# Kernel tuning notes

Hardware: AMD Instinct MI355X
Metric: run time of the kernel (lower is better)

The kernel has to match this reference:

```python
import jax, jax.numpy as jnp
import numpy as np

EMBED_SIZE = 1024
HEADS = 16
HEAD_DIM = EMBED_SIZE // HEADS


def setup_inputs() -> dict:
    key = jax.random.key(0)
    ks = jax.random.split(key, 8)
    B, S = 4, 2048
    inp = {
        "values": jax.random.normal(ks[0], (B, S, EMBED_SIZE), dtype=jnp.float32),
        "keys": jax.random.normal(ks[1], (B, S, EMBED_SIZE), dtype=jnp.float32),
        "query": jax.random.normal(ks[2], (B, S, EMBED_SIZE), dtype=jnp.float32),
        "mask": jnp.zeros((B, S), dtype=jnp.int32),  # accepted but unused, as in the original
        # per-head projection weights (nn.Linear(head_dim, head_dim, bias=False)): y = x @ W.T
        "Wv": jax.random.normal(ks[3], (HEAD_DIM, HEAD_DIM), dtype=jnp.float32) / np.sqrt(HEAD_DIM),
        "Wk": jax.random.normal(ks[4], (HEAD_DIM, HEAD_DIM), dtype=jnp.float32) / np.sqrt(HEAD_DIM),
        "Wq": jax.random.normal(ks[5], (HEAD_DIM, HEAD_DIM), dtype=jnp.float32) / np.sqrt(HEAD_DIM),
        # fc_out: nn.Linear(embed_size, embed_size)
        "Wo": jax.random.normal(ks[6], (EMBED_SIZE, EMBED_SIZE), dtype=jnp.float32) / np.sqrt(EMBED_SIZE),
        "bo": jax.random.normal(ks[7], (EMBED_SIZE,), dtype=jnp.float32) * 0.01,
    }
    return inp


def reference(values, keys, query, mask, Wv, Wk, Wq, Wo, bo):
    N, S, _ = query.shape
    # reshape to (N, len, heads, head_dim)
    v = values.reshape(N, S, HEADS, HEAD_DIM)
    k = keys.reshape(N, S, HEADS, HEAD_DIM)
    q = query.reshape(N, S, HEADS, HEAD_DIM)
    # per-head linear projections (shared across heads), y = x @ W.T
    v = jnp.einsum('nlhd,ed->nlhe', v, Wv)
    k = jnp.einsum('nlhd,ed->nlhe', k, Wk)
    q = jnp.einsum('nlhd,ed->nlhe', q, Wq)
    # attention scores: (N, H, Q, K), scaled by sqrt(embed_size) as in the original
    energy = jnp.einsum('nqhd,nkhd->nhqk', q, k)
    attention = jax.nn.softmax(energy / jnp.sqrt(jnp.float32(EMBED_SIZE)), axis=3)
    out = jnp.einsum('nhql,nlhd->nqhd', attention, v).reshape(N, S, EMBED_SIZE)
    out = out @ Wo.T + bo
    return out
```

## Files before the change

### kernel.cpp

```cpp
#include <hip/hip_runtime.h>


typedef __attribute__((ext_vector_type(8))) short short8;
typedef __attribute__((ext_vector_type(4))) float f32x4;
typedef __attribute__((ext_vector_type(2))) unsigned int uint2v;

constexpr int Bn = 4, Sn = 2048, Hn = 16, Dn = 64, En = 1024;
constexpr int HEADELEMS = Bn * Hn * Sn * Dn;

__device__ __forceinline__ unsigned short f2bf(float f) {
  union { float f; unsigned u; } x; x.f = f;
  unsigned u = x.u;
  return (unsigned short)((u + 0x7FFFu + ((u >> 16) & 1u)) >> 16);
}

__device__ __forceinline__ short8 pack8(f32x4 a, f32x4 b) {
  short8 r;
  r[0] = (short)f2bf(a[0]); r[1] = (short)f2bf(a[1]);
  r[2] = (short)f2bf(a[2]); r[3] = (short)f2bf(a[3]);
  r[4] = (short)f2bf(b[0]); r[5] = (short)f2bf(b[1]);
  r[6] = (short)f2bf(b[2]); r[7] = (short)f2bf(b[3]);
  return r;
}

__device__ __forceinline__ float fexp2(float x) {
#if __has_builtin(__builtin_amdgcn_exp2f)
  return __builtin_amdgcn_exp2f(x);
#else
  return exp2f(x);
#endif
}

__device__ __forceinline__ unsigned cvtpk_bf16(float lo, float hi) {
  unsigned r;
  asm("v_cvt_pk_bf16_f32 %0, %1, %2" : "=v"(r) : "v"(lo), "v"(hi));
  return r;
}

__device__ __forceinline__ void gload_lds16(const unsigned short* g, unsigned short* l) {
  __builtin_amdgcn_global_load_lds((const __attribute__((address_space(1))) void*)g,
                                   (__attribute__((address_space(3))) void*)l, 16, 0, 0);
}

__global__ __launch_bounds__(256) void wfused_kernel(
    const float* __restrict__ Wq, const float* __restrict__ Wk,
    const float* __restrict__ Wv, const float* __restrict__ Wo,
    unsigned short* __restrict__ Ut, unsigned short* __restrict__ Mg) {
  __shared__ float lv[4096];
  const int e = blockIdx.x, t = threadIdx.x;
  for (int i = t; i < 4096; i += 256) lv[i] = Wv[i];
  __syncthreads();
#pragma unroll
  for (int i = 0; i < 4; ++i) {
    int hd = i * 256 + t;
    int h = hd >> 6, d = hd & 63;
    float acc = 0.f;
    const float* wrow = Wo + e * 1024 + h * 64;
    for (int dp = 0; dp < 64; ++dp) acc += lv[dp * 64 + d] * wrow[dp];
    Ut[e * 1024 + hd] = f2bf(acc);
  }
  if (e < 16) {
    int idx = e * 256 + t;
    int d = idx >> 6, c = idx & 63;
    float acc = 0.f;
    for (int o = 0; o < 64; ++o) acc += Wq[o * 64 + d] * Wk[o * 64 + c];
    Mg[idx] = f2bf(acc * 0.04508422f);
  }
}

__global__ __launch_bounds__(256) void prep_kernel(
    const float* __restrict__ vin, const float* __restrict__ kin,
    const unsigned short* __restrict__ Mg,
    unsigned short* __restrict__ kp, unsigned short* __restrict__ vT) {
  __shared__ alignas(16) unsigned short ldsK[64][72];
  __shared__ alignas(16) unsigned short ldsV[64][72];

  const int blk = blockIdx.x;
  const int st = blk & 31, h = (blk >> 5) & 15, b = blk >> 9;
  const int s0 = st * 64;
  const int t = threadIdx.x;
  const int wid = t >> 6, lane = t & 63, lg = lane >> 4, li = lane & 15;
  const int row = t >> 2, seg = t & 3;
  const int srcoff = (b * Sn + s0 + row) * En + h * 64 + seg * 16;

  {
    const f32x4* ks = reinterpret_cast<const f32x4*>(kin + srcoff);
    *reinterpret_cast<short8*>(&ldsK[row][seg * 16]) = pack8(ks[0], ks[1]);
    *reinterpret_cast<short8*>(&ldsK[row][seg * 16 + 8]) = pack8(ks[2], ks[3]);
    const f32x4* vs = reinterpret_cast<const f32x4*>(vin + srcoff);
    *reinterpret_cast<short8*>(&ldsV[row][seg * 16]) = pack8(vs[0], vs[1]);
    *reinterpret_cast<short8*>(&ldsV[row][seg * 16 + 8]) = pack8(vs[2], vs[3]);
  }
  __syncthreads();

  {
    const int d = lane, sq = wid;
    unsigned short col[16];
#pragma unroll
    for (int j = 0; j < 16; ++j) col[j] = ldsV[sq * 16 + j][d];
    short8 o0, o1;
#pragma unroll
    for (int j = 0; j < 8; ++j) { o0[j] = (short)col[j]; o1[j] = (short)col[8 + j]; }
    unsigned short* dst = vT + ((size_t)((b * Hn + h) * Dn + d)) * Sn + s0 + sq * 16;
    *reinterpret_cast<short8*>(dst) = o0;
    *reinterpret_cast<short8*>(dst + 8) = o1;
  }

  {
    short8 ka0 = *reinterpret_cast<const short8*>(&ldsK[wid * 16 + li][lg * 8]);
    short8 ka1 = *reinterpret_cast<const short8*>(&ldsK[wid * 16 + li][32 + lg * 8]);
    f32x4 acc[4] = {{0,0,0,0},{0,0,0,0},{0,0,0,0},{0,0,0,0}};
#pragma unroll
    for (int cb = 0; cb < 4; ++cb) {
      short8 b0 = *reinterpret_cast<const short8*>(Mg + (cb * 16 + li) * 64 + lg * 8);
      short8 b1 = *reinterpret_cast<const short8*>(Mg + (cb * 16 + li) * 64 + 32 + lg * 8);
      acc[cb] = __builtin_amdgcn_mfma_f32_16x16x32_bf16(ka0, b0, acc[cb], 0, 0, 0);
      acc[cb] = __builtin_amdgcn_mfma_f32_16x16x32_bf16(ka1, b1, acc[cb], 0, 0, 0);
    }
#pragma unroll
    for (int cb = 0; cb < 4; ++cb)
#pragma unroll
      for (int r = 0; r < 4; ++r)
        ldsK[wid * 16 + lg * 4 + r][cb * 16 + li] = f2bf(acc[cb][r]);
  }
  __syncthreads();

  {
    unsigned short* dst = kp + ((size_t)((b * Hn + h) * Sn + s0 + row)) * Dn + seg * 16;
    *reinterpret_cast<short8*>(dst) = *reinterpret_cast<const short8*>(&ldsK[row][seg * 16]);
    *reinterpret_cast<short8*>(dst + 8) = *reinterpret_cast<const short8*>(&ldsK[row][seg * 16 + 8]);
  }
}

__global__ __launch_bounds__(512, 4) void attn_kernel(
    const float* __restrict__ qin, const unsigned short* __restrict__ kp,
    const unsigned short* __restrict__ vT, unsigned short* __restrict__ pv) {
  __shared__ alignas(16) unsigned short ldsK[2][4096];
  __shared__ alignas(16) unsigned short ldsV[2][4096];
  __shared__ alignas(16) unsigned short ldsP[8][32][72];

  const int bid = blockIdx.x;
  const int xcd = bid & 7, j = bid >> 3;
  const int bh = ((j & 7) << 3) + xcd;
  const int qt = j >> 3;
  const int b = bh >> 4, h = bh & 15;

  const int t = threadIdx.x;
  const int wid = t >> 6, lane = t & 63, lg = lane >> 4, li = lane & 15;
  const int bhS = bh * Sn;
  const int q0 = qt * 256 + wid * 32;

  const int koff0 = ((lg ^ (li & 7)) << 3);

  const int sr = t >> 3, sg = t & 7;
  const unsigned short* ksrc = kp + (size_t)(bhS + sr) * Dn + ((sg ^ (sr & 7)) << 3);
  const unsigned short* vsrc = vT + ((size_t)bh * Dn + sr) * Sn + ((sg ^ (sr & 7)) << 3);

  short8 qb[2][2];
#pragma unroll
  for (int rb = 0; rb < 2; ++rb)
#pragma unroll
    for (int kc = 0; kc < 2; ++kc) {
      const float* qrow = qin + (size_t)(b * Sn + q0 + rb * 16 + li) * En + h * 64 + kc * 32 + lg * 8;
      f32x4 a = *reinterpret_cast<const f32x4*>(qrow);
      f32x4 c = *reinterpret_cast<const f32x4*>(qrow + 4);
      qb[rb][kc] = pack8(a, c);
    }

  f32x4 o[2][4];
#pragma unroll
  for (int rb = 0; rb < 2; ++rb)
#pragma unroll
    for (int i = 0; i < 4; ++i) o[rb][i] = f32x4{0, 0, 0, 0};
  float l0 = 0.f, l1 = 0.f;

  auto stage = [&](int buf, int kt) {
    gload_lds16(ksrc + (size_t)kt * 4096, &ldsK[buf][t * 8]);
    gload_lds16(vsrc + kt * 64, &ldsV[buf][t * 8]);
  };

  stage(0, 0);
  __syncthreads();
  int cur = 0;

  for (int kt = 0; kt < 32; ++kt) {
    if (kt < 31) stage(cur ^ 1, kt + 1);

    const unsigned short* Kb = ldsK[cur];
#pragma unroll
    for (int cb = 0; cb < 4; ++cb) {
      const int ra = (cb * 16 + li) * 64 + koff0;
      short8 ka0 = *reinterpret_cast<const short8*>(&Kb[ra]);
      short8 ka1 = *reinterpret_cast<const short8*>(&Kb[ra ^ 32]);
      f32x4 s0 = {0, 0, 0, 0}, s1 = {0, 0, 0, 0};
      s0 = __builtin_amdgcn_mfma_f32_16x16x32_bf16(ka0, qb[0][0], s0, 0, 0, 0);
      s0 = __builtin_amdgcn_mfma_f32_16x16x32_bf16(ka1, qb[0][1], s0, 0, 0, 0);
      s1 = __builtin_amdgcn_mfma_f32_16x16x32_bf16(ka0, qb[1][0], s1, 0, 0, 0);
      s1 = __builtin_amdgcn_mfma_f32_16x16x32_bf16(ka1, qb[1][1], s1, 0, 0, 0);
      float p0[4], p1[4];
#pragma unroll
      for (int r = 0; r < 4; ++r) {
        p0[r] = fexp2(s0[r]); l0 += p0[r];
        p1[r] = fexp2(s1[r]); l1 += p1[r];
      }
      uint2v w0, w1;
      w0[0] = cvtpk_bf16(p0[0], p0[1]); w0[1] = cvtpk_bf16(p0[2], p0[3]);
      w1[0] = cvtpk_bf16(p1[0], p1[1]); w1[1] = cvtpk_bf16(p1[2], p1[3]);
      *reinterpret_cast<uint2v*>(&ldsP[wid][li][cb * 16 + 4 * lg]) = w0;
      *reinterpret_cast<uint2v*>(&ldsP[wid][16 + li][cb * 16 + 4 * lg]) = w1;
    }

    short8 pa[2][2];
#pragma unroll
    for (int rb = 0; rb < 2; ++rb)
#pragma unroll
      for (int kc = 0; kc < 2; ++kc)
        pa[rb][kc] = *reinterpret_cast<const short8*>(
            &ldsP[wid][rb * 16 + li][kc * 32 + lg * 8]);

    const unsigned short* Vb = ldsV[cur];
#pragma unroll
    for (int db = 0; db < 4; ++db) {
      const int va = (db * 16 + li) * 64 + koff0;
      short8 vb0 = *reinterpret_cast<const short8*>(&Vb[va]);
      short8 vb1 = *reinterpret_cast<const short8*>(&Vb[va ^ 32]);
      o[0][db] = __builtin_amdgcn_mfma_f32_16x16x32_bf16(pa[0][0], vb0, o[0][db], 0, 0, 0);
      o[0][db] = __builtin_amdgcn_mfma_f32_16x16x32_bf16(pa[0][1], vb1, o[0][db], 0, 0, 0);
      o[1][db] = __builtin_amdgcn_mfma_f32_16x16x32_bf16(pa[1][0], vb0, o[1][db], 0, 0, 0);
      o[1][db] = __builtin_amdgcn_mfma_f32_16x16x32_bf16(pa[1][1], vb1, o[1][db], 0, 0, 0);
    }

    __syncthreads();
    cur ^= 1;
  }

  l0 += __shfl_xor(l0, 16, 64); l0 += __shfl_xor(l0, 32, 64);
  l1 += __shfl_xor(l1, 16, 64); l1 += __shfl_xor(l1, 32, 64);
#pragma unroll
  for (int r = 0; r < 4; ++r) {
    float i0 = 1.f / __shfl(l0, 4 * lg + r, 16);
    float i1 = 1.f / __shfl(l1, 4 * lg + r, 16);
    const int sg2 = q0 + 4 * lg + r;
    unsigned short* d0 = pv + ((size_t)(b * Sn + sg2) * Hn + h) * Dn + li;
    unsigned short* d1 = d0 + (size_t)16 * Hn * Dn;
#pragma unroll
    for (int db = 0; db < 4; ++db) {
      d0[db * 16] = f2bf(o[0][db][r] * i0);
      d1[db * 16] = f2bf(o[1][db][r] * i1);
    }
  }
}

__global__ __launch_bounds__(256) void ogemm_kernel(
    const unsigned short* __restrict__ pvm, const unsigned short* __restrict__ Ut,
    const float* __restrict__ bo, float* __restrict__ out) {
  __shared__ alignas(16) unsigned short ldsA[2][8192];
  __shared__ alignas(16) unsigned short ldsB[2][8192];

  const int bid = blockIdx.x;
  const int wg = (bid & 7) * 64 + (bid >> 3);
  const int en = wg & 7, mt = wg >> 3;
  const int t = threadIdx.x;
  const int wid = t >> 6, lane = t & 63, lg = lane >> 4, li = lane & 15;
  const int wr = wid >> 1, wc = wid & 1;
  const int m0 = mt * 128, e0 = en * 128;

  f32x4 acc[4][4];
#pragma unroll
  for (int i = 0; i < 4; ++i)
#pragma unroll
    for (int jj = 0; jj < 4; ++jj) acc[i][jj] = f32x4{0, 0, 0, 0};

  const int r0 = t >> 3, G = t & 7;

  auto stage = [&](int buf, int k0) {
#pragma unroll
    for (int rd = 0; rd < 4; ++rd) {
      const int r = r0 + rd * 32;
      const int so = ((G ^ (r & 7)) << 3);
      gload_lds16(pvm + (size_t)(m0 + r) * 1024 + k0 + so, &ldsA[buf][rd * 2048 + t * 8]);
      gload_lds16(Ut + (size_t)(e0 + r) * 1024 + k0 + so, &ldsB[buf][rd * 2048 + t * 8]);
    }
  };

  stage(0, 0);
  __syncthreads();
  int cur = 0;

  for (int kt = 0; kt < 16; ++kt) {
    if (kt < 15) stage(cur ^ 1, (kt + 1) * 64);
#pragma unroll
    for (int kc = 0; kc < 2; ++kc) {
      short8 af[4], bfr[4];
#pragma unroll
      for (int mr = 0; mr < 4; ++mr) {
        const int row = wr * 64 + mr * 16 + li;
        af[mr] = *reinterpret_cast<const short8*>(
            &ldsA[cur][row * 64 + (((kc * 4 + lg) ^ (li & 7)) << 3)]);
      }
#pragma unroll
      for (int nr = 0; nr < 4; ++nr) {
        const int row = wc * 64 + nr * 16 + li;
        bfr[nr] = *reinterpret_cast<const short8*>(
            &ldsB[cur][row * 64 + (((kc * 4 + lg) ^ (li & 7)) << 3)]);
      }
#pragma unroll
      for (int mr = 0; mr < 4; ++mr)
#pragma unroll
        for (int nr = 0; nr < 4; ++nr)
          acc[mr][nr] = __builtin_amdgcn_mfma_f32_16x16x32_bf16(af[mr], bfr[nr], acc[mr][nr], 0, 0, 0);
    }
    __syncthreads();
    cur ^= 1;
  }

#pragma unroll
  for (int nr = 0; nr < 4; ++nr) {
    const int col = e0 + wc * 64 + nr * 16 + li;
    const float bias = bo[col];
#pragma unroll
    for (int mr = 0; mr < 4; ++mr)
#pragma unroll
      for (int r = 0; r < 4; ++r)
        out[(size_t)(m0 + wr * 64 + mr * 16 + lg * 4 + r) * 1024 + col] = acc[mr][nr][r] + bias;
  }
}

extern "C" void kernel_launch(void* const* d_in, const int* in_sizes, int n_in,
                              void* d_out, int out_size, void* d_ws, size_t ws_size,
                              hipStream_t stream) {
  const float* vin = (const float*)d_in[0];
  const float* kin = (const float*)d_in[1];
  const float* qin = (const float*)d_in[2];
  const float* Wv = (const float*)d_in[4];
  const float* Wk = (const float*)d_in[5];
  const float* Wq = (const float*)d_in[6];
  const float* Wo = (const float*)d_in[7];
  const float* bo = (const float*)d_in[8];
  float* out = (float*)d_out;

  unsigned short* kp = (unsigned short*)d_ws;
  unsigned short* vT = kp + HEADELEMS;
  unsigned short* pv = vT + HEADELEMS;
  unsigned short* Ut = pv + HEADELEMS;
  unsigned short* Mg = Ut + En * En;

  wfused_kernel<<<1024, 256, 0, stream>>>(Wq, Wk, Wv, Wo, Ut, Mg);
  prep_kernel<<<2048, 256, 0, stream>>>(vin, kin, Mg, kp, vT);
  attn_kernel<<<512, 512, 0, stream>>>(qin, kp, vT, pv);
  ogemm_kernel<<<512, 256, 0, stream>>>(pv, Ut, bo, out);
}
```

Baseline: 274.2 us.

## Switch attention to 32x32x16 MFMA with register-resident P via permlane swap

The attention kernel now uses 32x32x16 bf16 MFMAs, computing scores transposed so the exponentiated probabilities can be packed and rearranged with v_permlane32_swap into the A operand of the PV MFMA. This removes the per-warp LDS round trip for P. MFMA sections are wrapped in s_setprio to favour matrix issue, and the row-sum reduction becomes a single cross-half shuffle followed by an LDS broadcast of the inverse. The weight-folding kernel also now handles four output rows per block, with Wo staged in LDS, so it launches fewer blocks.

```diff
diff --git a/kernel.cpp b/kernel.cpp
--- a/kernel.cpp
+++ b/kernel.cpp
@@ -3,7 +3,8 @@
 
 typedef __attribute__((ext_vector_type(8))) short short8;
 typedef __attribute__((ext_vector_type(4))) float f32x4;
-typedef __attribute__((ext_vector_type(2))) unsigned int uint2v;
+typedef __attribute__((ext_vector_type(16))) float f32x16;
+typedef __attribute__((ext_vector_type(4))) unsigned int uint4v;
 
 constexpr int Bn = 4, Sn = 2048, Hn = 16, Dn = 64, En = 1024;
 constexpr int HEADELEMS = Bn * Hn * Sn * Dn;
@@ -42,27 +43,37 @@
                                    (__attribute__((address_space(3))) void*)l, 16, 0, 0);
 }
 
-__global__ __launch_bounds__(256) void wfused_kernel(
+__global__ __launch_bounds__(256) void wvo_kernel(
     const float* __restrict__ Wq, const float* __restrict__ Wk,
     const float* __restrict__ Wv, const float* __restrict__ Wo,
     unsigned short* __restrict__ Ut, unsigned short* __restrict__ Mg) {
   __shared__ float lv[4096];
-  const int e = blockIdx.x, t = threadIdx.x;
-  for (int i = t; i < 4096; i += 256) lv[i] = Wv[i];
-  __syncthreads();
-#pragma unroll
-  for (int i = 0; i < 4; ++i) {
-    int hd = i * 256 + t;
-    int h = hd >> 6, d = hd & 63;
+  __shared__ float lwo[4][1024];
+  const int bi = blockIdx.x, t = threadIdx.x;
+  const int e0 = bi * 4;
+  for (int i = t; i < 4096; i += 256) {
+    lv[i] = Wv[i];
+    lwo[i >> 10][i & 1023] = Wo[e0 * 1024 + i];
+  }
+  __syncthreads();
+  const int lane = t & 63, wid = t >> 6;
+#pragma unroll
+  for (int e = 0; e < 4; ++e) {
+#pragma unroll
+    for (int i = 0; i < 4; ++i) {
+      const int h = i * 4 + wid, d = lane;
+      float acc = 0.f;
+      const float* wrow = &lwo[e][h * 64];
+#pragma unroll 8
+      for (int dp = 0; dp < 64; ++dp) acc += lv[dp * 64 + d] * wrow[dp];
+      Ut[(size_t)(e0 + e) * 1024 + h * 64 + d] = f2bf(acc);
+    }
+  }
+  if (bi < 16) {
+    const int idx = bi * 256 + t;
+    const int d = idx >> 6, c = idx & 63;
     float acc = 0.f;
-    const float* wrow = Wo + e * 1024 + h * 64;
-    for (int dp = 0; dp < 64; ++dp) acc += lv[dp * 64 + d] * wrow[dp];
-    Ut[e * 1024 + hd] = f2bf(acc);
-  }
-  if (e < 16) {
-    int idx = e * 256 + t;
-    int d = idx >> 6, c = idx & 63;
-    float acc = 0.f;
+#pragma unroll 8
     for (int o = 0; o < 64; ++o) acc += Wq[o * 64 + d] * Wk[o * 64 + c];
     Mg[idx] = f2bf(acc * 0.04508422f);
   }
@@ -97,10 +108,10 @@
     const int d = lane, sq = wid;
     unsigned short col[16];
 #pragma unroll
-    for (int j = 0; j < 16; ++j) col[j] = ldsV[sq * 16 + j][d];
+    for (int jj = 0; jj < 16; ++jj) col[jj] = ldsV[sq * 16 + jj][d];
     short8 o0, o1;
 #pragma unroll
-    for (int j = 0; j < 8; ++j) { o0[j] = (short)col[j]; o1[j] = (short)col[8 + j]; }
+    for (int jj = 0; jj < 8; ++jj) { o0[jj] = (short)col[jj]; o1[jj] = (short)col[8 + jj]; }
     unsigned short* dst = vT + ((size_t)((b * Hn + h) * Dn + d)) * Sn + s0 + sq * 16;
     *reinterpret_cast<short8*>(dst) = o0;
     *reinterpret_cast<short8*>(dst + 8) = o1;
@@ -137,7 +148,7 @@
     const unsigned short* __restrict__ vT, unsigned short* __restrict__ pv) {
   __shared__ alignas(16) unsigned short ldsK[2][4096];
   __shared__ alignas(16) unsigned short ldsV[2][4096];
-  __shared__ alignas(16) unsigned short ldsP[8][32][72];
+  __shared__ float ldsL[8][32];
 
   const int bid = blockIdx.x;
   const int xcd = bid & 7, j = bid >> 3;
@@ -146,33 +157,28 @@
   const int b = bh >> 4, h = bh & 15;
 
   const int t = threadIdx.x;
-  const int wid = t >> 6, lane = t & 63, lg = lane >> 4, li = lane & 15;
+  const int wid = t >> 6, lane = t & 63;
+  const int c32 = lane & 31, hi = lane >> 5, rx = c32 & 7;
   const int bhS = bh * Sn;
   const int q0 = qt * 256 + wid * 32;
-
-  const int koff0 = ((lg ^ (li & 7)) << 3);
 
   const int sr = t >> 3, sg = t & 7;
   const unsigned short* ksrc = kp + (size_t)(bhS + sr) * Dn + ((sg ^ (sr & 7)) << 3);
   const unsigned short* vsrc = vT + ((size_t)bh * Dn + sr) * Sn + ((sg ^ (sr & 7)) << 3);
 
-  short8 qb[2][2];
-#pragma unroll
-  for (int rb = 0; rb < 2; ++rb)
-#pragma unroll
-    for (int kc = 0; kc < 2; ++kc) {
-      const float* qrow = qin + (size_t)(b * Sn + q0 + rb * 16 + li) * En + h * 64 + kc * 32 + lg * 8;
-      f32x4 a = *reinterpret_cast<const f32x4*>(qrow);
-      f32x4 c = *reinterpret_cast<const f32x4*>(qrow + 4);
-      qb[rb][kc] = pack8(a, c);
-    }
-
-  f32x4 o[2][4];
-#pragma unroll
-  for (int rb = 0; rb < 2; ++rb)
-#pragma unroll
-    for (int i = 0; i < 4; ++i) o[rb][i] = f32x4{0, 0, 0, 0};
-  float l0 = 0.f, l1 = 0.f;
+  short8 qb[4];
+#pragma unroll
+  for (int ks = 0; ks < 4; ++ks) {
+    const float* qrow = qin + (size_t)(b * Sn + q0 + c32) * En + h * 64 + ks * 16 + hi * 8;
+    f32x4 a = *reinterpret_cast<const f32x4*>(qrow);
+    f32x4 c = *reinterpret_cast<const f32x4*>(qrow + 4);
+    qb[ks] = pack8(a, c);
+  }
+
+  f32x16 o0, o1;
+#pragma unroll
+  for (int r = 0; r < 16; ++r) { o0[r] = 0.f; o1[r] = 0.f; }
+  float l = 0.f;
 
   auto stage = [&](int buf, int kt) {
     gload_lds16(ksrc + (size_t)kt * 4096, &ldsK[buf][t * 8]);
@@ -187,67 +193,75 @@
     if (kt < 31) stage(cur ^ 1, kt + 1);
 
     const unsigned short* Kb = ldsK[cur];
-#pragma unroll
-    for (int cb = 0; cb < 4; ++cb) {
-      const int ra = (cb * 16 + li) * 64 + koff0;
-      short8 ka0 = *reinterpret_cast<const short8*>(&Kb[ra]);
-      short8 ka1 = *reinterpret_cast<const short8*>(&Kb[ra ^ 32]);
-      f32x4 s0 = {0, 0, 0, 0}, s1 = {0, 0, 0, 0};
-      s0 = __builtin_amdgcn_mfma_f32_16x16x32_bf16(ka0, qb[0][0], s0, 0, 0, 0);
-      s0 = __builtin_amdgcn_mfma_f32_16x16x32_bf16(ka1, qb[0][1], s0, 0, 0, 0);
-      s1 = __builtin_amdgcn_mfma_f32_16x16x32_bf16(ka0, qb[1][0], s1, 0, 0, 0);
-      s1 = __builtin_amdgcn_mfma_f32_16x16x32_bf16(ka1, qb[1][1], s1, 0, 0, 0);
-      float p0[4], p1[4];
-#pragma unroll
-      for (int r = 0; r < 4; ++r) {
-        p0[r] = fexp2(s0[r]); l0 += p0[r];
-        p1[r] = fexp2(s1[r]); l1 += p1[r];
+    f32x16 s0, s1;
+#pragma unroll
+    for (int r = 0; r < 16; ++r) { s0[r] = 0.f; s1[r] = 0.f; }
+    __builtin_amdgcn_s_setprio(1);
+#pragma unroll
+    for (int ks = 0; ks < 4; ++ks) {
+      const int ch = (((2 * ks + hi) ^ rx) << 3);
+      short8 ka0 = *reinterpret_cast<const short8*>(&Kb[c32 * 64 + ch]);
+      short8 ka1 = *reinterpret_cast<const short8*>(&Kb[(32 + c32) * 64 + ch]);
+      s0 = __builtin_amdgcn_mfma_f32_32x32x16_bf16(ka0, qb[ks], s0, 0, 0, 0);
+      s1 = __builtin_amdgcn_mfma_f32_32x32x16_bf16(ka1, qb[ks], s1, 0, 0, 0);
+    }
+    __builtin_amdgcn_s_setprio(0);
+
+#pragma unroll
+    for (int r = 0; r < 16; ++r) { s0[r] = fexp2(s0[r]); l += s0[r]; }
+#pragma unroll
+    for (int r = 0; r < 16; ++r) { s1[r] = fexp2(s1[r]); l += s1[r]; }
+
+    short8 pa[4];
+#pragma unroll
+    for (int s2 = 0; s2 < 2; ++s2) {
+      {
+        unsigned k0 = cvtpk_bf16(s0[8 * s2 + 0], s0[8 * s2 + 1]);
+        unsigned k1 = cvtpk_bf16(s0[8 * s2 + 2], s0[8 * s2 + 3]);
+        unsigned k2 = cvtpk_bf16(s0[8 * s2 + 4], s0[8 * s2 + 5]);
+        unsigned k3 = cvtpk_bf16(s0[8 * s2 + 6], s0[8 * s2 + 7]);
+        asm("v_permlane32_swap_b32 %0, %1" : "+v"(k0), "+v"(k2));
+        asm("v_permlane32_swap_b32 %0, %1" : "+v"(k1), "+v"(k3));
+        uint4v u; u[0] = k0; u[1] = k1; u[2] = k2; u[3] = k3;
+        pa[s2] = __builtin_bit_cast(short8, u);
       }
-      uint2v w0, w1;
-      w0[0] = cvtpk_bf16(p0[0], p0[1]); w0[1] = cvtpk_bf16(p0[2], p0[3]);
-      w1[0] = cvtpk_bf16(p1[0], p1[1]); w1[1] = cvtpk_bf16(p1[2], p1[3]);
-      *reinterpret_cast<uint2v*>(&ldsP[wid][li][cb * 16 + 4 * lg]) = w0;
-      *reinterpret_cast<uint2v*>(&ldsP[wid][16 + li][cb * 16 + 4 * lg]) = w1;
-    }
-
-    short8 pa[2][2];
-#pragma unroll
-    for (int rb = 0; rb < 2; ++rb)
-#pragma unroll
-      for (int kc = 0; kc < 2; ++kc)
-        pa[rb][kc] = *reinterpret_cast<const short8*>(
-            &ldsP[wid][rb * 16 + li][kc * 32 + lg * 8]);
+      {
+        unsigned k0 = cvtpk_bf16(s1[8 * s2 + 0], s1[8 * s2 + 1]);
+        unsigned k1 = cvtpk_bf16(s1[8 * s2 + 2], s1[8 * s2 + 3]);
+        unsigned k2 = cvtpk_bf16(s1[8 * s2 + 4], s1[8 * s2 + 5]);
+        unsigned k3 = cvtpk_bf16(s1[8 * s2 + 6], s1[8 * s2 + 7]);
+        asm("v_permlane32_swap_b32 %0, %1" : "+v"(k0), "+v"(k2));
+        asm("v_permlane32_swap_b32 %0, %1" : "+v"(k1), "+v"(k3));
+        uint4v u; u[0] = k0; u[1] = k1; u[2] = k2; u[3] = k3;
+        pa[2 + s2] = __builtin_bit_cast(short8, u);
+      }
+    }
 
     const unsigned short* Vb = ldsV[cur];
-#pragma unroll
-    for (int db = 0; db < 4; ++db) {
-      const int va = (db * 16 + li) * 64 + koff0;
-      short8 vb0 = *reinterpret_cast<const short8*>(&Vb[va]);
-      short8 vb1 = *reinterpret_cast<const short8*>(&Vb[va ^ 32]);
-      o[0][db] = __builtin_amdgcn_mfma_f32_16x16x32_bf16(pa[0][0], vb0, o[0][db], 0, 0, 0);
-      o[0][db] = __builtin_amdgcn_mfma_f32_16x16x32_bf16(pa[0][1], vb1, o[0][db], 0, 0, 0);
-      o[1][db] = __builtin_amdgcn_mfma_f32_16x16x32_bf16(pa[1][0], vb0, o[1][db], 0, 0, 0);
-      o[1][db] = __builtin_amdgcn_mfma_f32_16x16x32_bf16(pa[1][1], vb1, o[1][db], 0, 0, 0);
-    }
+    __builtin_amdgcn_s_setprio(1);
+#pragma unroll
+    for (int ks2 = 0; ks2 < 4; ++ks2) {
+      const int ch = (((2 * ks2 + hi) ^ rx) << 3);
+      short8 vb0 = *reinterpret_cast<const short8*>(&Vb[c32 * 64 + ch]);
+      short8 vb1 = *reinterpret_cast<const short8*>(&Vb[(32 + c32) * 64 + ch]);
+      o0 = __builtin_amdgcn_mfma_f32_32x32x16_bf16(pa[ks2], vb0, o0, 0, 0, 0);
+      o1 = __builtin_amdgcn_mfma_f32_32x32x16_bf16(pa[ks2], vb1, o1, 0, 0, 0);
+    }
+    __builtin_amdgcn_s_setprio(0);
 
     __syncthreads();
     cur ^= 1;
   }
 
-  l0 += __shfl_xor(l0, 16, 64); l0 += __shfl_xor(l0, 32, 64);
-  l1 += __shfl_xor(l1, 16, 64); l1 += __shfl_xor(l1, 32, 64);
-#pragma unroll
-  for (int r = 0; r < 4; ++r) {
-    float i0 = 1.f / __shfl(l0, 4 * lg + r, 16);
-    float i1 = 1.f / __shfl(l1, 4 * lg + r, 16);
-    const int sg2 = q0 + 4 * lg + r;
-    unsigned short* d0 = pv + ((size_t)(b * Sn + sg2) * Hn + h) * Dn + li;
-    unsigned short* d1 = d0 + (size_t)16 * Hn * Dn;
-#pragma unroll
-    for (int db = 0; db < 4; ++db) {
-      d0[db * 16] = f2bf(o[0][db][r] * i0);
-      d1[db * 16] = f2bf(o[1][db][r] * i1);
-    }
+  l += __shfl_xor(l, 32, 64);
+  ldsL[wid][c32] = 1.f / l;
+#pragma unroll
+  for (int r = 0; r < 16; ++r) {
+    const int ql = (r & 3) + 8 * (r >> 2) + 4 * hi;
+    const float inv = ldsL[wid][ql];
+    unsigned short* dst = pv + ((size_t)(b * Sn + q0 + ql) * Hn + h) * Dn + c32;
+    dst[0]  = f2bf(o0[r] * inv);
+    dst[32] = f2bf(o1[r] * inv);
   }
 }
 
@@ -345,7 +359,7 @@
   unsigned short* Ut = pv + HEADELEMS;
   unsigned short* Mg = Ut + En * En;
 
-  wfused_kernel<<<1024, 256, 0, stream>>>(Wq, Wk, Wv, Wo, Ut, Mg);
+  wvo_kernel<<<256, 256, 0, stream>>>(Wq, Wk, Wv, Wo, Ut, Mg);
   prep_kernel<<<2048, 256, 0, stream>>>(vin, kin, Mg, kp, vT);
   attn_kernel<<<512, 512, 0, stream>>>(qin, kp, vT, pv);
   ogemm_kernel<<<512, 256, 0, stream>>>(pv, Ut, bo, out);
```

Result: no change. 268.9 us (-1.9%).
